# Kernel optimization log

Hardware: AMD Instinct MI355X
Metric: run time of the kernel (lower is better)

## Reference

```python
import jax, jax.numpy as jnp
import numpy as np

B, H, S, D = 2, 16, 2048, 128
SPARSITY = 0.1
NEG = -1.0e9


def local_mask(seq_len: int) -> jnp.ndarray:
    # window_size = max(1, int(seq_len * sparsity)); row i keeps cols [i-w//2, i+w//2]
    w = max(1, int(seq_len * SPARSITY))
    half = w // 2
    idx = jnp.arange(seq_len)
    diff = idx[None, :] - idx[:, None]  # j - i
    return ((diff >= -half) & (diff <= half)).astype(jnp.float32)


def setup_inputs() -> dict:
    key = jax.random.key(0)
    kq, kk, kv = jax.random.split(key, 3)
    return {
        "query": jax.random.normal(kq, (B, H, S, D), dtype=jnp.float32),
        "key": jax.random.normal(kk, (B, H, S, D), dtype=jnp.float32),
        "value": jax.random.normal(kv, (B, H, S, D), dtype=jnp.float32),
    }


def reference(query, key, value):
    head_dim = query.shape[-1]
    seq_len_k = key.shape[2]
    m = local_mask(seq_len_k)[None, None]  # [1,1,S,S]
    scores = jnp.einsum("bhqd,bhkd->bhqk", query, key) / jnp.sqrt(
        jnp.asarray(head_dim, query.dtype)
    )
    scores = scores * m + (1.0 - m) * NEG
    probs = jax.nn.softmax(scores, axis=-1)
    context = jnp.einsum("bhqk,bhkd->bhqd", probs, value)
    return context, probs
```

## Files before the change

### kernel.cpp

```cpp
#include <hip/hip_runtime.h>
#include <math.h>


namespace {
constexpr int Sc = 2048, Dc = 128;
constexpr int HALFW = 102;
constexpr float SCALE = 0.08838834764831845f;
constexpr int TQ  = 32;
constexpr int CT  = 256;
constexpr int KST = 136;
constexpr int VST = 132;
constexpr int PTS = 36;
constexpr int OFF_PST = 0;
constexpr int OFF_VSF = 18432;
constexpr int SLAB    = 35328;
constexpr int OFF_RED = SLAB;
constexpr int LDS_TOTAL = SLAB + 512 + 128 + 128;
}

typedef __bf16 bf16x8 __attribute__((ext_vector_type(8)));
typedef float  f32x16 __attribute__((ext_vector_type(16)));
typedef float  fx4    __attribute__((ext_vector_type(4)));
typedef unsigned short u16x8 __attribute__((ext_vector_type(8)));
typedef unsigned short u16x4 __attribute__((ext_vector_type(4)));

__device__ __forceinline__ unsigned short f2bf(float f) {
    unsigned u = __float_as_uint(f);
    u += 0x7fffu + ((u >> 16) & 1u);
    return (unsigned short)(u >> 16);
}
__device__ __forceinline__ float bf2f(unsigned short h) {
    return __uint_as_float(((unsigned)h) << 16);
}
__device__ __forceinline__ void bar_lds() {
    asm volatile("s_waitcnt lgkmcnt(0)\n\ts_barrier" ::: "memory");
}

__global__ __launch_bounds__(256, 4) void sparse_attn_mfma(
    const float* __restrict__ Q, const float* __restrict__ K,
    const float* __restrict__ V, float* __restrict__ ctx,
    float* __restrict__ probs)
{
    __shared__ __align__(16) unsigned char smem[LDS_TOTAL];
    unsigned short* Ks   = (unsigned short*)(smem);
    unsigned short* Ps_t = (unsigned short*)(smem + OFF_PST);
    float*          Vsf  = (float*)(smem + OFF_VSF);
    float (*red)[4]      = (float(*)[4])(smem + OFF_RED);
    float* rowM          = (float*)(smem + OFF_RED + 512);
    float* rowSinv       = (float*)(smem + OFF_RED + 512 + 128);

    const int tid  = threadIdx.x;
    const int lane = tid & 63;
    const int w    = tid >> 6;
    const int lo   = lane & 31;
    const int hi   = lane >> 5;

    const int wid = (blockIdx.x & 7) * 256 + (blockIdx.x >> 3);
    const int bh  = wid >> 6;
    const int qt  = wid & 63;
    const int i0  = qt * TQ;
    const int js0 = max(0, i0 - HALFW);
    const int jend = min(js0 + CT, Sc);

    const size_t rowbase = (size_t)bh * Sc;
    float* probsBase = probs + (rowbase + i0) * (size_t)Sc;

    const float4* K4 = (const float4*)(K + rowbase * Dc);
    const float4* V4 = (const float4*)(V + rowbase * Dc);

    bf16x8 aq[8];
    {
        const float4* Q4 = (const float4*)(Q + (rowbase + i0) * Dc);
        #pragma unroll 2
        for (int dk = 0; dk < 8; ++dk) {
            float4 a = Q4[lo * 32 + dk * 4 + hi * 2];
            float4 b = Q4[lo * 32 + dk * 4 + hi * 2 + 1];
            u16x8 t;
            t[0] = f2bf(a.x); t[1] = f2bf(a.y); t[2] = f2bf(a.z); t[3] = f2bf(a.w);
            t[4] = f2bf(b.x); t[5] = f2bf(b.y); t[6] = f2bf(b.z); t[7] = f2bf(b.w);
            aq[dk] = __builtin_bit_cast(bf16x8, t);
        }
    }

    f32x16 accE[2];
    #pragma unroll
    for (int ch = 0; ch < 2; ++ch) {
        #pragma unroll 4
        for (int it = 0; it < 16; ++it) {
            int idx = tid + 256 * it;
            int r = idx >> 5, d4 = idx & 31;
            int jn = js0 + ch * 128 + r;
            if (jn > Sc - 1) jn = Sc - 1;
            float4 k4 = K4[(size_t)jn * 32 + d4];
            ushort4 b;
            b.x = f2bf(k4.x); b.y = f2bf(k4.y); b.z = f2bf(k4.z); b.w = f2bf(k4.w);
            *(ushort4*)&Ks[r * KST + d4 * 4] = b;
        }
        bar_lds();
        f32x16 acc;
        #pragma unroll
        for (int i = 0; i < 16; ++i) acc[i] = 0.0f;
        const unsigned short* krow = &Ks[(w * 32 + lo) * KST + hi * 8];
        #pragma unroll
        for (int dk = 0; dk < 8; ++dk) {
            bf16x8 b = *(const bf16x8*)(krow + dk * 16);
            acc = __builtin_amdgcn_mfma_f32_32x32x16_bf16(aq[dk], b, acc, 0, 0, 0);
        }
        accE[ch] = acc;
        bar_lds();
    }

    const int cg0 = js0 + w * 32 + lo;
    {
        float mred[16];
        #pragma unroll
        for (int i = 0; i < 16; ++i) {
            int rl = (i & 3) + 8 * (i >> 2) + 4 * hi;
            int rg = i0 + rl;
            float m = -3.0e38f;
            #pragma unroll
            for (int ch = 0; ch < 2; ++ch) {
                int cg = cg0 + ch * 128;
                bool valid = (cg < Sc) & (cg >= rg - HALFW) & (cg <= rg + HALFW);
                float sv = valid ? accE[ch][i] * SCALE : -3.0e38f;
                accE[ch][i] = sv;
                m = fmaxf(m, sv);
            }
            mred[i] = m;
        }
        #pragma unroll
        for (int mk = 1; mk < 32; mk <<= 1) {
            #pragma unroll
            for (int i = 0; i < 16; ++i)
                mred[i] = fmaxf(mred[i], __shfl_xor(mred[i], mk, 64));
        }
        if (lo == 0) {
            #pragma unroll
            for (int i = 0; i < 16; ++i) {
                int rl = (i & 3) + 8 * (i >> 2) + 4 * hi;
                red[rl][w] = mred[i];
            }
        }
    }
    bar_lds();
    if (tid < 128) {
        int rr = tid >> 2, sl = tid & 3;
        float v = red[rr][sl];
        v = fmaxf(v, __shfl_xor(v, 1, 64));
        v = fmaxf(v, __shfl_xor(v, 2, 64));
        if (sl == 0) rowM[rr] = v;
    }
    bar_lds();

    {
        float sred[16];
        #pragma unroll
        for (int i = 0; i < 16; ++i) {
            int rl = (i & 3) + 8 * (i >> 2) + 4 * hi;
            float rm = rowM[rl];
            float e0 = __expf(accE[0][i] - rm);
            float e1 = __expf(accE[1][i] - rm);
            accE[0][i] = e0; accE[1][i] = e1;
            sred[i] = e0 + e1;
        }
        #pragma unroll
        for (int mk = 1; mk < 32; mk <<= 1) {
            #pragma unroll
            for (int i = 0; i < 16; ++i)
                sred[i] += __shfl_xor(sred[i], mk, 64);
        }
        if (lo == 0) {
            #pragma unroll
            for (int i = 0; i < 16; ++i) {
                int rl = (i & 3) + 8 * (i >> 2) + 4 * hi;
                red[rl][w] = sred[i];
            }
        }
    }
    bar_lds();
    if (tid < 128) {
        int rr = tid >> 2, sl = tid & 3;
        float v = red[rr][sl];
        v += __shfl_xor(v, 1, 64);
        v += __shfl_xor(v, 2, 64);
        if (sl == 0) rowSinv[rr] = 1.0f / v;
    }
    bar_lds();

    #pragma unroll
    for (int i = 0; i < 16; ++i) {
        int rl = (i & 3) + 8 * (i >> 2) + 4 * hi;
        float inv = rowSinv[rl];
        float* prow = probsBase + (size_t)rl * Sc;
        #pragma unroll
        for (int ch = 0; ch < 2; ++ch) {
            int cg = cg0 + ch * 128;
            float p = accE[ch][i] * inv;
            Ps_t[(cg - js0) * PTS + rl] = f2bf(p);
            if (cg < Sc) __builtin_nontemporal_store(p, prow + cg);
        }
    }
    bar_lds();

    const int kp  = lane & 3;
    const int dgq = (lane >> 2) & 1;
    const int rg  = lane >> 3;
    fx4 o[4][4];
    #pragma unroll
    for (int c = 0; c < 4; ++c)
        #pragma unroll
        for (int j = 0; j < 4; ++j) o[c][j] = (fx4){0.f, 0.f, 0.f, 0.f};

    #pragma unroll 2
    for (int ch8 = 0; ch8 < 8; ++ch8) {
        #pragma unroll
        for (int it = 0; it < 4; ++it) {
            int idx = tid + 256 * it;
            int r = idx >> 5, d4 = idx & 31;
            int jn = js0 + ch8 * 32 + r;
            if (jn > Sc - 1) jn = Sc - 1;
            float4 v4g = V4[(size_t)jn * 32 + d4];
            *(float4*)&Vsf[r * VST + d4 * 4] = v4g;
        }
        bar_lds();
        const unsigned short* Pbase = &Ps_t[(ch8 * 32) * PTS + 4 * rg];
        const float* Vbase = &Vsf[w * 32 + dgq * 16];
        #pragma unroll 4
        for (int kk = 0; kk < 8; ++kk) {
            int k = 4 * kk + kp;
            u16x4 pb = *(const u16x4*)(Pbase + k * PTS);
            const float* vr = Vbase + k * VST;
            fx4 v0 = *(const fx4*)(vr);
            fx4 v1 = *(const fx4*)(vr + 4);
            fx4 v2 = *(const fx4*)(vr + 8);
            fx4 v3 = *(const fx4*)(vr + 12);
            #pragma unroll
            for (int c = 0; c < 4; ++c) {
                float pc = bf2f(pb[c]);
                o[c][0] += v0 * pc;
                o[c][1] += v1 * pc;
                o[c][2] += v2 * pc;
                o[c][3] += v3 * pc;
            }
        }
        bar_lds();
    }

    #pragma unroll
    for (int c = 0; c < 4; ++c) {
        #pragma unroll
        for (int j = 0; j < 4; ++j) {
            fx4 t = o[c][j];
            #pragma unroll
            for (int comp = 0; comp < 4; ++comp) {
                float s = t[comp];
                s += __shfl_xor(s, 1, 64);
                s += __shfl_xor(s, 2, 64);
                t[comp] = s;
            }
            o[c][j] = t;
        }
    }
    if (kp == 0) {
        #pragma unroll
        for (int c = 0; c < 4; ++c) {
            float* crow = ctx + (rowbase + i0 + 4 * rg + c) * (size_t)Dc
                        + w * 32 + dgq * 16;
            #pragma unroll
            for (int j = 0; j < 4; ++j)
                __builtin_nontemporal_store(o[c][j], (fx4*)crow + j);
        }
    }

    {
        const int headN = js0 & 3;
        const int tailN = (4 - (jend & 3)) & 3;
        const int hn = headN + tailN;
        if (hn == 4) {
            int r = tid >> 2, s = tid & 3;
            if (r < TQ) {
                int col = (s < headN) ? (js0 - headN + s) : (jend + s - headN);
                __builtin_nontemporal_store(0.0f, probsBase + (size_t)r * Sc + col);
            }
        } else if (hn == 2) {
            int r = tid >> 1, s = tid & 1;
            if (r < TQ) {
                int col = (s < headN) ? (js0 - headN + s) : (jend + s - headN);
                __builtin_nontemporal_store(0.0f, probsBase + (size_t)r * Sc + col);
            }
        }
        const int leftQ   = (js0 - headN) >> 2;
        const int rightQ0 = (jend + tailN) >> 2;
        const fx4 z4 = {0.f, 0.f, 0.f, 0.f};
        for (int r = 0; r < TQ; ++r) {
            fx4* p4 = (fx4*)(probsBase + (size_t)r * Sc);
            for (int c = tid; c < leftQ; c += 256)
                __builtin_nontemporal_store(z4, p4 + c);
            for (int c = rightQ0 + tid; c < Sc / 4; c += 256)
                __builtin_nontemporal_store(z4, p4 + c);
        }
    }
}

extern "C" void kernel_launch(void* const* d_in, const int* in_sizes, int n_in,
                              void* d_out, int out_size, void* d_ws, size_t ws_size,
                              hipStream_t stream) {
    const float* Q = (const float*)d_in[0];
    const float* K = (const float*)d_in[1];
    const float* V = (const float*)d_in[2];
    float* out   = (float*)d_out;
    float* ctx   = out;
    float* probs = out + (size_t)2 * 16 * 2048 * 128;

    dim3 grid(2 * 16 * (Sc / TQ));
    dim3 block(256);
    sparse_attn_mfma<<<grid, block, 0, stream>>>(Q, K, V, ctx, probs);
}
```

Measured before the change: 797.0 us.

## Zero probs with hipMemsetAsync and stage V in 64-row chunks

The in-kernel zero-fill of the probs matrix outside each tile's band is removed. The whole probs buffer is now cleared by a hipMemsetAsync before the kernel, and the kernel writes only the band values. V staging is widened from 32-row to 64-row chunks, so there are half as many barriers, at the cost of a larger LDS slab and occupancy lowered to 3 blocks. The memset writes the full 512MB buffer, including the band region that the kernel then writes again, so it adds redundant write traffic and a second launch.

```diff
diff --git a/kernel.cpp b/kernel.cpp
--- a/kernel.cpp
+++ b/kernel.cpp
@@ -13,7 +13,7 @@
 constexpr int PTS = 36;
 constexpr int OFF_PST = 0;
 constexpr int OFF_VSF = 18432;
-constexpr int SLAB    = 35328;
+constexpr int SLAB    = 52224;
 constexpr int OFF_RED = SLAB;
 constexpr int LDS_TOTAL = SLAB + 512 + 128 + 128;
 }
@@ -36,7 +36,7 @@
     asm volatile("s_waitcnt lgkmcnt(0)\n\ts_barrier" ::: "memory");
 }
 
-__global__ __launch_bounds__(256, 4) void sparse_attn_mfma(
+__global__ __launch_bounds__(256, 3) void sparse_attn_mfma(
     const float* __restrict__ Q, const float* __restrict__ K,
     const float* __restrict__ V, float* __restrict__ ctx,
     float* __restrict__ probs)
@@ -60,7 +60,6 @@
     const int qt  = wid & 63;
     const int i0  = qt * TQ;
     const int js0 = max(0, i0 - HALFW);
-    const int jend = min(js0 + CT, Sc);
 
     const size_t rowbase = (size_t)bh * Sc;
     float* probsBase = probs + (rowbase + i0) * (size_t)Sc;
@@ -211,22 +210,22 @@
         #pragma unroll
         for (int j = 0; j < 4; ++j) o[c][j] = (fx4){0.f, 0.f, 0.f, 0.f};
 
-    #pragma unroll 2
-    for (int ch8 = 0; ch8 < 8; ++ch8) {
-        #pragma unroll
-        for (int it = 0; it < 4; ++it) {
+    #pragma unroll 1
+    for (int ch4 = 0; ch4 < 4; ++ch4) {
+        #pragma unroll
+        for (int it = 0; it < 8; ++it) {
             int idx = tid + 256 * it;
             int r = idx >> 5, d4 = idx & 31;
-            int jn = js0 + ch8 * 32 + r;
+            int jn = js0 + ch4 * 64 + r;
             if (jn > Sc - 1) jn = Sc - 1;
             float4 v4g = V4[(size_t)jn * 32 + d4];
             *(float4*)&Vsf[r * VST + d4 * 4] = v4g;
         }
         bar_lds();
-        const unsigned short* Pbase = &Ps_t[(ch8 * 32) * PTS + 4 * rg];
+        const unsigned short* Pbase = &Ps_t[(ch4 * 64) * PTS + 4 * rg];
         const float* Vbase = &Vsf[w * 32 + dgq * 16];
         #pragma unroll 4
-        for (int kk = 0; kk < 8; ++kk) {
+        for (int kk = 0; kk < 16; ++kk) {
             int k = 4 * kk + kp;
             u16x4 pb = *(const u16x4*)(Pbase + k * PTS);
             const float* vr = Vbase + k * VST;
@@ -269,35 +268,6 @@
             #pragma unroll
             for (int j = 0; j < 4; ++j)
                 __builtin_nontemporal_store(o[c][j], (fx4*)crow + j);
-        }
-    }
-
-    {
-        const int headN = js0 & 3;
-        const int tailN = (4 - (jend & 3)) & 3;
-        const int hn = headN + tailN;
-        if (hn == 4) {
-            int r = tid >> 2, s = tid & 3;
-            if (r < TQ) {
-                int col = (s < headN) ? (js0 - headN + s) : (jend + s - headN);
-                __builtin_nontemporal_store(0.0f, probsBase + (size_t)r * Sc + col);
-            }
-        } else if (hn == 2) {
-            int r = tid >> 1, s = tid & 1;
-            if (r < TQ) {
-                int col = (s < headN) ? (js0 - headN + s) : (jend + s - headN);
-                __builtin_nontemporal_store(0.0f, probsBase + (size_t)r * Sc + col);
-            }
-        }
-        const int leftQ   = (js0 - headN) >> 2;
-        const int rightQ0 = (jend + tailN) >> 2;
-        const fx4 z4 = {0.f, 0.f, 0.f, 0.f};
-        for (int r = 0; r < TQ; ++r) {
-            fx4* p4 = (fx4*)(probsBase + (size_t)r * Sc);
-            for (int c = tid; c < leftQ; c += 256)
-                __builtin_nontemporal_store(z4, p4 + c);
-            for (int c = rightQ0 + tid; c < Sc / 4; c += 256)
-                __builtin_nontemporal_store(z4, p4 + c);
         }
     }
 }
@@ -312,6 +282,9 @@
     float* ctx   = out;
     float* probs = out + (size_t)2 * 16 * 2048 * 128;
 
+    const size_t probsBytes = (size_t)2 * 16 * 2048 * 2048 * sizeof(float);
+    hipMemsetAsync(probs, 0, probsBytes, stream);
+
     dim3 grid(2 * 16 * (Sc / TQ));
     dim3 block(256);
     sparse_attn_mfma<<<grid, block, 0, stream>>>(Q, K, V, ctx, probs);
```

Measured after the change: 818.0 us. 1.03x slower.
